# Optimization experiments

Measured on AMD Instinct MI355X. Metric: run time of the kernel, lower is better.

The kernel has to match this reference:

```python
import jax, jax.numpy as jnp
import numpy as np

D = 2048          # n_embd
H = 4 * D         # hidden_size
B, S = 4, 2048


def _make_masks(seed=0):
    rng = np.random.default_rng(seed)
    # mask1: for each group of 4 output rows, keep 2 of 4 rows (whole rows)
    mask1 = np.zeros((H, D), dtype=np.float32)
    for i in range(0, H, 4):
        keep = rng.permutation(4)[:2] + i
        mask1[keep, :] = 1.0
    # mask2: for each group of 4 input columns, keep 2 of 4 columns
    mask2 = np.zeros((D, H), dtype=np.float32)
    for i in range(0, H, 4):
        keep = rng.permutation(4)[:2] + i
        mask2[:, keep] = 1.0
    return jnp.asarray(mask1), jnp.asarray(mask2)


def setup_inputs() -> dict:
    key = jax.random.key(0)
    k_x, k_w1, k_w2 = jax.random.split(key, 3)
    x = jax.random.normal(k_x, (B, S, D), dtype=jnp.float32)
    # Kaiming-uniform-ish init like nn.Linear defaults
    w1 = jax.random.uniform(k_w1, (H, D), dtype=jnp.float32, minval=-1.0, maxval=1.0) / np.sqrt(D)
    w2 = jax.random.uniform(k_w2, (D, H), dtype=jnp.float32, minval=-1.0, maxval=1.0) / np.sqrt(H)
    mask1, mask2 = _make_masks()
    return {"x": x, "w1": w1, "w2": w2, "mask1": mask1, "mask2": mask2}


def reference(x, w1, w2, mask1, mask2):
    # sparse_multiply is elementwise mask application on the weights
    sw1 = w1 * mask1                      # [H, D]
    sw2 = w2 * mask2                      # [D, H]
    h = jnp.einsum('bsd,hd->bsh', x, sw1) # F.linear(x, sw1)
    h = jax.nn.gelu(h, approximate=False) # torch F.gelu default = exact erf
    out = jnp.einsum('bsh,dh->bsd', h, sw2)
    return out
```

## Files before the change

kernel.cpp:

```cpp
#include <hip/hip_runtime.h>
#include <hip/hip_bf16.h>

typedef __bf16 bf16_t;
typedef __bf16 bf16x8 __attribute__((ext_vector_type(8)));
typedef float f32x4 __attribute__((ext_vector_type(4)));

__device__ __forceinline__ unsigned short f32_to_bf16_rn(float f) {
  unsigned u = __float_as_uint(f);
  u += 0x7fffu + ((u >> 16) & 1u);
  return (unsigned short)(u >> 16);
}

__device__ __forceinline__ ushort4 cvt4(float4 v) {
  ushort4 o;
  o.x = f32_to_bf16_rn(v.x);
  o.y = f32_to_bf16_rn(v.y);
  o.z = f32_to_bf16_rn(v.z);
  o.w = f32_to_bf16_rn(v.w);
  return o;
}

__device__ __forceinline__ float gelu_exact(float x) {
  return 0.5f * x * (1.0f + erff(x * 0.7071067811865475f));
}

#define GLDS16(g, l)                                                          \
  __builtin_amdgcn_global_load_lds(                                           \
      (const __attribute__((address_space(1))) void*)(g),                     \
      (__attribute__((address_space(3))) void*)(l), 16, 0, 0)

__global__ void build_idx_kernel(const float* __restrict__ mask1,
                                 const float* __restrict__ mask2,
                                 int* __restrict__ idx, int* __restrict__ meta,
                                 int H, int D) {
  __shared__ int sums[1024];
  const int t = threadIdx.x;
  int flags[8];
  int tot = 0;
#pragma unroll
  for (int u = 0; u < 8; ++u) {
    int j = t * 8 + u;
    int f = (mask1[(long long)j * D] != 0.0f) && (mask2[j] != 0.0f);
    flags[u] = f;
    tot += f;
  }
  sums[t] = tot;
  __syncthreads();
  for (int off = 1; off < 1024; off <<= 1) {
    int v = (t >= off) ? sums[t - off] : 0;
    __syncthreads();
    sums[t] += v;
    __syncthreads();
  }
  int pos = sums[t] - tot;
#pragma unroll
  for (int u = 0; u < 8; ++u) {
    if (flags[u]) idx[pos++] = t * 8 + u;
  }
  if (t == 1023) {
    int count = sums[1023];
    meta[0] = count;
    meta[1] = (count + 127) & ~127;
  }
}

__global__ void prep_kernel(const float* __restrict__ x,
                            const float* __restrict__ w1,
                            const float* __restrict__ w2,
                            const int* __restrict__ idx,
                            const int* __restrict__ meta,
                            unsigned short* __restrict__ xb,
                            unsigned short* __restrict__ w1c,
                            unsigned short* __restrict__ w2c, int D, int H) {
  const int nx = 4194304;
  const int count = meta[0];
  const int kpad = meta[1];
  const int nw1 = kpad << 9;
  const int nw2 = 2097152;
  const int total = nx + nw1 + nw2;
  for (int i = blockIdx.x * 256 + threadIdx.x; i < total; i += 2048 * 256) {
    if (i < nx) {
      ((ushort4*)xb)[i] = cvt4(((const float4*)x)[i]);
    } else if (i < nx + nw1) {
      int q = i - nx;
      int k = q >> 9;
      int d4 = (q & 511) << 2;
      ushort4 o = {0, 0, 0, 0};
      if (k < count)
        o = cvt4(*(const float4*)(w1 + (long long)idx[k] * D + d4));
      *(ushort4*)(w1c + (long long)k * D + d4) = o;
    } else {
      int q = i - nx - nw1;
      int n = q >> 10;
      int k4 = (q & 1023) << 2;
      ushort4 o = {0, 0, 0, 0};
      const float* src = w2 + (long long)n * H;
#pragma unroll
      for (int u = 0; u < 4; ++u) {
        int k = k4 + u;
        unsigned short v = 0;
        if (k < count) v = f32_to_bf16_rn(src[idx[k]]);
        ((unsigned short*)&o)[u] = v;
      }
      *(ushort4*)(w2c + (long long)n * 4096 + k4) = o;
    }
  }
}

template <int EPI>
__global__ __launch_bounds__(256, 4) void gemm_pool_kernel(
    const bf16_t* __restrict__ A, const bf16_t* __restrict__ B,
    void* __restrict__ Cout, long long ldA, long long ldB, long long ldC,
    int Kfix, int ncolFix, const int* __restrict__ meta) {
  const int kpad = meta[1];
  const int K = (EPI == 0) ? kpad : Kfix;
  const int ncol = (EPI == 1) ? (kpad >> 7) : ncolFix;
  const int ntiles = ncol << 6;
  const int NT = K >> 6;
  const int phase = ((blockIdx.x >> 8) & 3) * (NT >> 2);

  __shared__ bf16_t As[128 * 64];
  __shared__ bf16_t Bs[128 * 64];

  const int tid = threadIdx.x;
  const int l = tid & 63;
  const int w = tid >> 6;
  const int wm = w >> 1;
  const int wn = w & 1;

  const int srow = tid >> 3;
  const int sg = ((tid & 7) ^ ((tid >> 3) & 7)) * 8;

  const int fr = l & 15;
  const int gA = (l >> 4) ^ (l & 7);

  for (int tau = blockIdx.x; tau < ntiles; tau += gridDim.x) {
    const int row = tau & 63;
    const int col = tau >> 6;
    const long long brow = (long long)row * 128;
    const long long bcol = (long long)col * 128;

    const bf16_t* Ag = A + (brow + srow) * ldA + sg;
    const bf16_t* Bg = B + (bcol + srow) * ldB + sg;

    f32x4 acc[4][4];
#pragma unroll
    for (int m = 0; m < 4; ++m)
#pragma unroll
      for (int n = 0; n < 4; ++n) acc[m][n] = (f32x4){0.f, 0.f, 0.f, 0.f};

    for (int it = 0; it < NT; ++it) {
      int t = it + phase;
      if (t >= NT) t -= NT;
      const int k0 = t << 6;
      GLDS16(Ag + k0, &As[tid * 8]);
      GLDS16(Ag + 32 * ldA + k0, &As[2048 + tid * 8]);
      GLDS16(Ag + 64 * ldA + k0, &As[4096 + tid * 8]);
      GLDS16(Ag + 96 * ldA + k0, &As[6144 + tid * 8]);
      GLDS16(Bg + k0, &Bs[tid * 8]);
      GLDS16(Bg + 32 * ldB + k0, &Bs[2048 + tid * 8]);
      GLDS16(Bg + 64 * ldB + k0, &Bs[4096 + tid * 8]);
      GLDS16(Bg + 96 * ldB + k0, &Bs[6144 + tid * 8]);
      __syncthreads();
#pragma unroll
      for (int kk = 0; kk < 2; ++kk) {
        const int gp = (gA ^ (kk * 4)) * 8;
        bf16x8 af[4], bfr[4];
#pragma unroll
        for (int m = 0; m < 4; ++m)
          af[m] = *(const bf16x8*)(&As[(wm * 64 + m * 16 + fr) * 64 + gp]);
#pragma unroll
        for (int n = 0; n < 4; ++n)
          bfr[n] = *(const bf16x8*)(&Bs[(wn * 64 + n * 16 + fr) * 64 + gp]);
#pragma unroll
        for (int m = 0; m < 4; ++m)
#pragma unroll
          for (int n = 0; n < 4; ++n)
            acc[m][n] = __builtin_amdgcn_mfma_f32_16x16x32_bf16(
                af[m], bfr[n], acc[m][n], 0, 0, 0);
      }
      __syncthreads();
    }

    const int orow = wm * 64 + (l >> 4) * 4;
    const int ocol = wn * 64 + fr;
#pragma unroll
    for (int m = 0; m < 4; ++m)
#pragma unroll
      for (int n = 0; n < 4; ++n)
#pragma unroll
        for (int r = 0; r < 4; ++r) {
          long long rr = brow + orow + m * 16 + r;
          long long cc = bcol + ocol + n * 16;
          float v = acc[m][n][r];
          if (EPI == 1) {
            ((unsigned short*)Cout)[rr * ldC + cc] =
                f32_to_bf16_rn(gelu_exact(v));
          } else {
            ((float*)Cout)[rr * ldC + cc] = v;
          }
        }
  }
}

extern "C" void kernel_launch(void* const* d_in, const int* in_sizes, int n_in,
                              void* d_out, int out_size, void* d_ws,
                              size_t ws_size, hipStream_t stream) {
  const float* x = (const float*)d_in[0];
  const float* w1 = (const float*)d_in[1];
  const float* w2 = (const float*)d_in[2];
  const float* mask1 = (const float*)d_in[3];
  const float* mask2 = (const float*)d_in[4];
  float* out = (float*)d_out;

  const int D = 2048, H = 8192, M = 8192;
  const int KP = 4096;

  char* ws = (char*)d_ws;
  unsigned short* xb = (unsigned short*)ws;
  unsigned short* w1c = xb + (size_t)M * D;
  unsigned short* w2c = w1c + (size_t)KP * D;
  unsigned short* hb = w2c + (size_t)D * KP;
  int* idx = (int*)(hb + (size_t)M * KP);
  int* meta = idx + KP;

  build_idx_kernel<<<1, 1024, 0, stream>>>(mask1, mask2, idx, meta, H, D);

  prep_kernel<<<2048, 256, 0, stream>>>(x, w1, w2, idx, meta, xb, w1c, w2c, D,
                                        H);

  gemm_pool_kernel<1><<<1024, 256, 0, stream>>>(
      (const bf16_t*)xb, (const bf16_t*)w1c, hb, (long long)D, (long long)D,
      (long long)KP, D, 0, meta);

  gemm_pool_kernel<0><<<1024, 256, 0, stream>>>(
      (const bf16_t*)hb, (const bf16_t*)w2c, out, (long long)KP,
      (long long)KP, (long long)D, 0, 16, meta);
}
```

Before: 240.7 us.

## Shrink GEMM tile to 128x64 and overlap x cast with mask index build

The GEMM block tile drops from 128x128 to 128x64, with 2048 blocks per GEMM and an 8-way K-phase stagger instead of 4-way. Each block loads less B per K step and holds fewer accumulators, which should raise occupancy and improve load balance. The cost is less arithmetic per byte loaded and more redundant loads of the A tile. Separately, the x-to-bf16 cast moves out of prep_kernel into the otherwise single-block index-building kernel, so the cast runs alongside the serial prefix scan.

```diff
diff --git a/kernel.cpp b/kernel.cpp
--- a/kernel.cpp
+++ b/kernel.cpp
@@ -29,68 +29,71 @@
       (const __attribute__((address_space(1))) void*)(g),                     \
       (__attribute__((address_space(3))) void*)(l), 16, 0, 0)
 
-__global__ void build_idx_kernel(const float* __restrict__ mask1,
-                                 const float* __restrict__ mask2,
-                                 int* __restrict__ idx, int* __restrict__ meta,
-                                 int H, int D) {
-  __shared__ int sums[1024];
-  const int t = threadIdx.x;
-  int flags[8];
-  int tot = 0;
-#pragma unroll
-  for (int u = 0; u < 8; ++u) {
-    int j = t * 8 + u;
-    int f = (mask1[(long long)j * D] != 0.0f) && (mask2[j] != 0.0f);
-    flags[u] = f;
-    tot += f;
+__global__ void build_and_cast_kernel(const float* __restrict__ mask1,
+                                      const float* __restrict__ mask2,
+                                      const float* __restrict__ x,
+                                      unsigned short* __restrict__ xb,
+                                      int* __restrict__ idx,
+                                      int* __restrict__ meta, int H, int D) {
+  if (blockIdx.x == 0) {
+    __shared__ int sums[1024];
+    const int t = threadIdx.x;
+    int flags[8];
+    int tot = 0;
+#pragma unroll
+    for (int u = 0; u < 8; ++u) {
+      int j = t * 8 + u;
+      int f = (mask1[(long long)j * D] != 0.0f) && (mask2[j] != 0.0f);
+      flags[u] = f;
+      tot += f;
+    }
+    sums[t] = tot;
+    __syncthreads();
+    for (int off = 1; off < 1024; off <<= 1) {
+      int v = (t >= off) ? sums[t - off] : 0;
+      __syncthreads();
+      sums[t] += v;
+      __syncthreads();
+    }
+    int pos = sums[t] - tot;
+#pragma unroll
+    for (int u = 0; u < 8; ++u) {
+      if (flags[u]) idx[pos++] = t * 8 + u;
+    }
+    if (t == 1023) {
+      int count = sums[1023];
+      meta[0] = count;
+      meta[1] = (count + 127) & ~127;
+    }
+  } else {
+    const int nx = 4194304;
+    for (int i = (blockIdx.x - 1) * 1024 + threadIdx.x; i < nx;
+         i += 512 * 1024)
+      ((ushort4*)xb)[i] = cvt4(((const float4*)x)[i]);
   }
-  sums[t] = tot;
-  __syncthreads();
-  for (int off = 1; off < 1024; off <<= 1) {
-    int v = (t >= off) ? sums[t - off] : 0;
-    __syncthreads();
-    sums[t] += v;
-    __syncthreads();
-  }
-  int pos = sums[t] - tot;
-#pragma unroll
-  for (int u = 0; u < 8; ++u) {
-    if (flags[u]) idx[pos++] = t * 8 + u;
-  }
-  if (t == 1023) {
-    int count = sums[1023];
-    meta[0] = count;
-    meta[1] = (count + 127) & ~127;
-  }
-}
-
-__global__ void prep_kernel(const float* __restrict__ x,
-                            const float* __restrict__ w1,
+}
+
+__global__ void prep_kernel(const float* __restrict__ w1,
                             const float* __restrict__ w2,
                             const int* __restrict__ idx,
                             const int* __restrict__ meta,
-                            unsigned short* __restrict__ xb,
                             unsigned short* __restrict__ w1c,
                             unsigned short* __restrict__ w2c, int D, int H) {
-  const int nx = 4194304;
   const int count = meta[0];
   const int kpad = meta[1];
   const int nw1 = kpad << 9;
   const int nw2 = 2097152;
-  const int total = nx + nw1 + nw2;
+  const int total = nw1 + nw2;
   for (int i = blockIdx.x * 256 + threadIdx.x; i < total; i += 2048 * 256) {
-    if (i < nx) {
-      ((ushort4*)xb)[i] = cvt4(((const float4*)x)[i]);
-    } else if (i < nx + nw1) {
-      int q = i - nx;
-      int k = q >> 9;
-      int d4 = (q & 511) << 2;
+    if (i < nw1) {
+      int k = i >> 9;
+      int d4 = (i & 511) << 2;
       ushort4 o = {0, 0, 0, 0};
       if (k < count)
         o = cvt4(*(const float4*)(w1 + (long long)idx[k] * D + d4));
       *(ushort4*)(w1c + (long long)k * D + d4) = o;
     } else {
-      int q = i - nx - nw1;
+      int q = i - nw1;
       int n = q >> 10;
       int k4 = (q & 1023) << 2;
       ushort4 o = {0, 0, 0, 0};
@@ -114,13 +117,13 @@
     int Kfix, int ncolFix, const int* __restrict__ meta) {
   const int kpad = meta[1];
   const int K = (EPI == 0) ? kpad : Kfix;
-  const int ncol = (EPI == 1) ? (kpad >> 7) : ncolFix;
+  const int ncol = (EPI == 1) ? (kpad >> 6) : ncolFix;
   const int ntiles = ncol << 6;
   const int NT = K >> 6;
-  const int phase = ((blockIdx.x >> 8) & 3) * (NT >> 2);
+  const int phase = (((blockIdx.x >> 8) & 7) * NT) >> 3;
 
   __shared__ bf16_t As[128 * 64];
-  __shared__ bf16_t Bs[128 * 64];
+  __shared__ bf16_t Bs[64 * 64];
 
   const int tid = threadIdx.x;
   const int l = tid & 63;
@@ -138,16 +141,16 @@
     const int row = tau & 63;
     const int col = tau >> 6;
     const long long brow = (long long)row * 128;
-    const long long bcol = (long long)col * 128;
+    const long long bcol = (long long)col * 64;
 
     const bf16_t* Ag = A + (brow + srow) * ldA + sg;
     const bf16_t* Bg = B + (bcol + srow) * ldB + sg;
 
-    f32x4 acc[4][4];
+    f32x4 acc[4][2];
 #pragma unroll
     for (int m = 0; m < 4; ++m)
 #pragma unroll
-      for (int n = 0; n < 4; ++n) acc[m][n] = (f32x4){0.f, 0.f, 0.f, 0.f};
+      for (int n = 0; n < 2; ++n) acc[m][n] = (f32x4){0.f, 0.f, 0.f, 0.f};
 
     for (int it = 0; it < NT; ++it) {
       int t = it + phase;
@@ -159,23 +162,21 @@
       GLDS16(Ag + 96 * ldA + k0, &As[6144 + tid * 8]);
       GLDS16(Bg + k0, &Bs[tid * 8]);
       GLDS16(Bg + 32 * ldB + k0, &Bs[2048 + tid * 8]);
-      GLDS16(Bg + 64 * ldB + k0, &Bs[4096 + tid * 8]);
-      GLDS16(Bg + 96 * ldB + k0, &Bs[6144 + tid * 8]);
       __syncthreads();
 #pragma unroll
       for (int kk = 0; kk < 2; ++kk) {
         const int gp = (gA ^ (kk * 4)) * 8;
-        bf16x8 af[4], bfr[4];
+        bf16x8 af[4], bfr[2];
 #pragma unroll
         for (int m = 0; m < 4; ++m)
           af[m] = *(const bf16x8*)(&As[(wm * 64 + m * 16 + fr) * 64 + gp]);
 #pragma unroll
-        for (int n = 0; n < 4; ++n)
-          bfr[n] = *(const bf16x8*)(&Bs[(wn * 64 + n * 16 + fr) * 64 + gp]);
+        for (int n = 0; n < 2; ++n)
+          bfr[n] = *(const bf16x8*)(&Bs[(wn * 32 + n * 16 + fr) * 64 + gp]);
 #pragma unroll
         for (int m = 0; m < 4; ++m)
 #pragma unroll
-          for (int n = 0; n < 4; ++n)
+          for (int n = 0; n < 2; ++n)
             acc[m][n] = __builtin_amdgcn_mfma_f32_16x16x32_bf16(
                 af[m], bfr[n], acc[m][n], 0, 0, 0);
       }
@@ -183,11 +184,11 @@
     }
 
     const int orow = wm * 64 + (l >> 4) * 4;
-    const int ocol = wn * 64 + fr;
+    const int ocol = wn * 32 + fr;
 #pragma unroll
     for (int m = 0; m < 4; ++m)
 #pragma unroll
-      for (int n = 0; n < 4; ++n)
+      for (int n = 0; n < 2; ++n)
 #pragma unroll
         for (int r = 0; r < 4; ++r) {
           long long rr = brow + orow + m * 16 + r;
@@ -224,16 +225,16 @@
   int* idx = (int*)(hb + (size_t)M * KP);
   int* meta = idx + KP;
 
-  build_idx_kernel<<<1, 1024, 0, stream>>>(mask1, mask2, idx, meta, H, D);
-
-  prep_kernel<<<2048, 256, 0, stream>>>(x, w1, w2, idx, meta, xb, w1c, w2c, D,
-                                        H);
-
-  gemm_pool_kernel<1><<<1024, 256, 0, stream>>>(
+  build_and_cast_kernel<<<513, 1024, 0, stream>>>(mask1, mask2, x, xb, idx,
+                                                  meta, H, D);
+
+  prep_kernel<<<2048, 256, 0, stream>>>(w1, w2, idx, meta, w1c, w2c, D, H);
+
+  gemm_pool_kernel<1><<<2048, 256, 0, stream>>>(
       (const bf16_t*)xb, (const bf16_t*)w1c, hb, (long long)D, (long long)D,
       (long long)KP, D, 0, meta);
 
-  gemm_pool_kernel<0><<<1024, 256, 0, stream>>>(
+  gemm_pool_kernel<0><<<2048, 256, 0, stream>>>(
       (const bf16_t*)hb, (const bf16_t*)w2c, out, (long long)KP,
-      (long long)KP, (long long)D, 0, 16, meta);
-}
+      (long long)KP, (long long)D, 0, 32, meta);
+}
```

Result: slower. 250.5 us (+4.1%).
